# Kernel tuning notes

Measured on AMD Instinct MI355X. Metric: run time of the kernel, lower is better.

The kernel has to match this reference:

```python
import jax, jax.numpy as jnp
from jax import lax
import numpy as np

K = 32          # PyG radius_graph default max_num_neighbors
NEG = -1e9      # mask fill for max-aggregation


def _gather(a, i):  # a [N,C], i [...,] int -> a[i]
    return a[i]


def radius_knn(pos, r):
    # pos [B,N,3] -> (idx [B,N,K], valid [B,N,K]) nearest-K within radius r, self excluded
    sq = jnp.sum(pos * pos, -1)                                   # [B,N]
    d2 = sq[:, :, None] + sq[:, None, :] - 2.0 * jnp.einsum('bnc,bmc->bnm', pos, pos)
    N = pos.shape[1]
    d2 = d2 + jnp.eye(N, dtype=pos.dtype) * 1e9                    # exclude self-loops
    neg, idx = lax.top_k(-d2, K)
    valid = (-neg) <= r * r
    return idx, valid


def fps(pos, n):
    # iterative farthest point sampling, deterministic start at index 0; pos [B,N,3] -> idx [B,n]
    def one(p):
        mind0 = jnp.sum((p - p[0]) ** 2, -1)
        def step(mind, _):
            i = jnp.argmax(mind)
            nd = jnp.sum((p - p[i]) ** 2, -1)
            return jnp.minimum(mind, nd), i
        _, idxs = lax.scan(step, mind0, None, length=n - 1)
        return jnp.concatenate([jnp.zeros((1,), jnp.int32), idxs.astype(jnp.int32)])
    return jax.vmap(one)(pos)


def point_conv(x, pos, idx, valid, W1, b1, W2, b2):
    # PyG PointNetConv: msg = local_nn(concat(x_j, pos_j - pos_i)), max-aggregate
    g = jax.vmap(_gather)
    rel = g(pos, idx) - pos[:, :, None, :]                         # [B,N,K,3]
    feat = rel if x is None else jnp.concatenate([g(x, idx), rel], -1)
    h = jax.nn.relu(feat @ W1 + b1) @ W2 + b2                      # [B,N,K,C]
    h = jnp.where(valid[..., None], h, NEG)
    return jnp.max(h, axis=2)                                      # [B,N,C]


def _forward(pos, W1a, b1a, W1b, b1b, W2a, b2a, W2b, b2b, W3a, b3a, W3b, b3b,
             Wc1, bc1, Wc2, bc2, Wc3, bc3, Wd1, bd1, Wd2, bd2):
    take = jax.vmap(_gather)
    B, N, _ = pos.shape
    idx, v = radius_knn(pos, 0.2)
    x = jax.nn.relu(point_conv(None, pos, idx, v, W1a, b1a, W1b, b1b))
    fi = fps(pos, N // 2)
    x, pos = take(x, fi), take(pos, fi)
    idx, v = radius_knn(pos, 0.4)
    x = jax.nn.relu(point_conv(x, pos, idx, v, W2a, b2a, W2b, b2b))
    fi = fps(pos, N // 8)
    x, pos = take(x, fi), take(pos, fi)
    idx, v = radius_knn(pos, 1.0)
    x = jax.nn.relu(point_conv(x, pos, idx, v, W3a, b3a, W3b, b3b))
    feat = jnp.max(x, axis=1)                                      # global max pool [B,256]
    h = jax.nn.relu(feat @ Wc1 + bc1)
    h = jax.nn.relu(h @ Wc2 + bc2)                                 # dropout is identity in eval
    logits = h @ Wc3 + bc3
    h2 = jax.nn.relu(feat @ Wd1 + bd1)
    d = h2 @ Wd2 + bd2
    return jax.nn.log_softmax(logits, axis=-1), jax.nn.log_softmax(d, axis=-1)


def setup_inputs() -> dict:
    key = jax.random.key(0)
    ks = jax.random.split(key, 32)
    def lin(k, fin, fout):
        kw, kb = jax.random.split(k)
        s = 1.0 / np.sqrt(fin)
        return (jax.random.uniform(kw, (fin, fout), jnp.float32, -s, s),
                jax.random.uniform(kb, (fout,), jnp.float32, -s, s))
    inp = {'pos': jax.random.uniform(ks[0], (8, 4096, 3), jnp.float32)}
    names = [('W1a','b1a',3,64),('W1b','b1b',64,64),('W2a','b2a',67,128),('W2b','b2b',128,128),
             ('W3a','b3a',131,256),('W3b','b3b',256,256),('Wc1','bc1',256,256),('Wc2','bc2',256,256),
             ('Wc3','bc3',256,40),('Wd1','bd1',256,256),('Wd2','bd2',256,2)]
    for i, (wn, bn, fin, fout) in enumerate(names):
        W, b = lin(ks[i + 1], fin, fout)
        inp[wn], inp[bn] = W, b
    return inp


def reference(pos, W1a, b1a, W1b, b1b, W2a, b2a, W2b, b2b, W3a, b3a, W3b, b3b,
              Wc1, bc1, Wc2, bc2, Wc3, bc3, Wd1, bd1, Wd2, bd2):
    return _forward(pos, W1a, b1a, W1b, b1b, W2a, b2a, W2b, b2b, W3a, b3a, W3b, b3b,
                    Wc1, bc1, Wc2, bc2, Wc3, bc3, Wd1, bd1, Wd2, bd2)
```

## Files before the change

### kernel.cpp

```cpp
#include <hip/hip_runtime.h>


#define NB 8

__device__ __forceinline__ unsigned obits(float f) {
  unsigned u = __float_as_uint(f);
  return (u & 0x80000000u) ? ~u : (u | 0x80000000u);
}

static constexpr int CAND = 1024;

template<int CTRL>
__device__ __forceinline__ unsigned long long dpp_max_step(unsigned long long v) {
  const int lo = (int)(unsigned)(v & 0xffffffffull);
  const int hi = (int)(unsigned)(v >> 32);
  const unsigned nlo = (unsigned)__builtin_amdgcn_update_dpp(lo, lo, CTRL, 0xf, 0xf, false);
  const unsigned nhi = (unsigned)__builtin_amdgcn_update_dpp(hi, hi, CTRL, 0xf, 0xf, false);
  const unsigned long long nv = ((unsigned long long)nhi << 32) | nlo;
  return (nv > v) ? nv : v;
}

__device__ __forceinline__ unsigned wave_iscan_add(unsigned x) {
  x += (unsigned)__builtin_amdgcn_update_dpp(0, (int)x, 0x111, 0xf, 0xf, true);
  x += (unsigned)__builtin_amdgcn_update_dpp(0, (int)x, 0x112, 0xf, 0xf, true);
  x += (unsigned)__builtin_amdgcn_update_dpp(0, (int)x, 0x114, 0xf, 0xf, true);
  x += (unsigned)__builtin_amdgcn_update_dpp(0, (int)x, 0x118, 0xf, 0xf, true);
  x += (unsigned)__builtin_amdgcn_update_dpp(0, (int)x, 0x142, 0xa, 0xf, true);
  x += (unsigned)__builtin_amdgcn_update_dpp(0, (int)x, 0x143, 0xc, 0xf, true);
  return x;
}

__device__ __forceinline__ unsigned long long u64max(unsigned long long a,
                                                    unsigned long long b) {
  return (b > a) ? b : a;
}

__device__ __forceinline__ void set_wave_prio_hi() {
#if __has_builtin(__builtin_amdgcn_s_setprio)
  __builtin_amdgcn_s_setprio(3);
#endif
}

__device__ __forceinline__ unsigned morton3_8(unsigned cx, unsigned cy, unsigned cz) {
  unsigned m = ((cx & 1u) << 2) | ((cy & 1u) << 1) | (cz & 1u);
  m |= ((cx & 2u) << 4) | ((cy & 2u) << 3) | ((cz & 2u) << 2);
  m |= ((cx & 4u) << 6) | ((cy & 4u) << 5) | ((cz & 4u) << 4);
  return m;
}

template<int N, int NOUT, int T>
__device__ __forceinline__ void fps_body(char* sm, const float* __restrict__ pb,
                                         int* __restrict__ fi, int b) {
  constexpr int P = N / T;
  constexpr int NW = T / 64;
  constexpr int CELLS = 512;
  constexpr int CH = NOUT;
  constexpr int NCHUNK = N / CH;
  static_assert(CH % P == 0 && N % CH == 0, "chunking");
  static_assert(CELLS <= T, "prefix scan needs CELLS <= T");
  int4* sPosI = (int4*)sm;
  int*  sfi   = (int*)(sm + (size_t)N * 16);
  unsigned long long* sKey =
      (unsigned long long*)(sm + (size_t)N * 16 + NOUT * 4);
  unsigned* hist = (unsigned*)(sm + (size_t)N * 16 + NOUT * 4 + 128);
  int* sOrd = sfi;
  const int tid = threadIdx.x, wid = tid >> 6, lane = tid & 63;
  set_wave_prio_hi();

  for (int t = tid; t < N; t += T) {
    sPosI[t] = make_int4((int)(pb[3*t]   * 8388608.f),
                         (int)(pb[3*t+1] * 8388608.f),
                         (int)(pb[3*t+2] * 8388608.f), 0);
  }
  for (int c = tid; c < CELLS; c += T) hist[c] = 0u;
  __syncthreads();

  unsigned myc[P];
#pragma unroll
  for (int r = 0; r < P; r++) {
    const int t = tid + r * T;
    const int4 p4 = sPosI[t];
    const unsigned cell = morton3_8((unsigned)p4.x >> 20,
                                    (unsigned)p4.y >> 20,
                                    (unsigned)p4.z >> 20);
    myc[r] = cell;
    atomicAdd(&hist[cell], 1u);
  }
  __syncthreads();

  {
    unsigned* sPart = (unsigned*)sKey;
    unsigned v = (tid < CELLS) ? hist[tid] : 0u;
    const unsigned isc = wave_iscan_add(v);
    if (lane == 63) sPart[wid] = isc;
    __syncthreads();
    unsigned offs = 0;
#pragma unroll
    for (int w2 = 0; w2 < NW; w2++) offs += (w2 < wid) ? sPart[w2] : 0u;
    if (tid < CELLS) hist[tid] = offs + isc - v;
    __syncthreads();
  }

  int myslot[P];
#pragma unroll
  for (int r = 0; r < P; r++) myslot[r] = (int)atomicAdd(&hist[myc[r]], 1u);

  int ex[P], ey[P], ez[P]; unsigned einv[P];
  for (int pc = 0; pc < NCHUNK; pc++) {
    __syncthreads();
#pragma unroll
    for (int r = 0; r < P; r++) {
      const int s = myslot[r];
      if (s >= pc * CH && s < (pc + 1) * CH) sOrd[s - pc * CH] = tid + r * T;
    }
    __syncthreads();
    if ((tid * P) / CH == pc) {
#pragma unroll
      for (int e = 0; e < P; e++) {
        const int o = sOrd[tid * P + e - pc * CH];
        const int4 p4 = sPosI[o];
        ex[e] = p4.x; ey[e] = p4.y; ez[e] = p4.z;
        einv[e] = (unsigned)(4095 - o);
      }
    }
  }
  __syncthreads();

  int lox = ex[0], hix = ex[0], loy = ey[0], hiy = ey[0], loz = ez[0], hiz = ez[0];
#pragma unroll
  for (int e = 1; e < P; e++) {
    lox = min(lox, ex[e]); hix = max(hix, ex[e]);
    loy = min(loy, ey[e]); hiy = max(hiy, ey[e]);
    loz = min(loz, ez[e]); hiz = max(hiz, ez[e]);
  }

  const int4 p0 = sPosI[0];
  unsigned long long mind[P];
  unsigned long long bv;
  {
    unsigned long long tv[P];
#pragma unroll
    for (int e = 0; e < P; e++) {
      const long long dx = ex[e] - p0.x, dy = ey[e] - p0.y, dz = ez[e] - p0.z;
      const unsigned long long d2 =
          (unsigned long long)(dx * dx + dy * dy + dz * dz);
      const unsigned long long k = (d2 << 12) | einv[e];
      mind[e] = k; tv[e] = k;
    }
#pragma unroll
    for (int s = 1; s < P; s <<= 1)
#pragma unroll
      for (int e = 0; e + s < P; e += 2 * s)
        if (tv[e + s] > tv[e]) tv[e] = tv[e + s];
    bv = tv[0];
  }
  if (tid == 0) sfi[0] = 0;

  for (int t = 1; t < NOUT; t++) {
    unsigned long long v = bv;
    v = dpp_max_step<0x111>(v);
    v = dpp_max_step<0x112>(v);
    v = dpp_max_step<0x114>(v);
    v = dpp_max_step<0x118>(v);
    v = dpp_max_step<0x142>(v);
    v = dpp_max_step<0x143>(v);
    const int pp = t & 1;
    if (lane == 63) sKey[pp * NW + wid] = v;
    __syncthreads();
    unsigned long long best;
    if (NW == 8) {
      const ulonglong2* sK2 = (const ulonglong2*)(sKey + pp * 8);
      const ulonglong2 a0 = sK2[0], a1 = sK2[1], a2 = sK2[2], a3 = sK2[3];
      best = u64max(u64max(u64max(a0.x, a0.y), u64max(a1.x, a1.y)),
                    u64max(u64max(a2.x, a2.y), u64max(a3.x, a3.y)));
    } else {
      unsigned long long k0 = sKey[pp*NW+0];
#pragma unroll
      for (int w2 = 1; w2 < NW; w2++) k0 = u64max(k0, sKey[pp*NW+w2]);
      best = k0;
    }
    const int ii = 4095 - (int)(best & 0xFFFull);
    if (tid == 0) sfi[t] = ii;
    const int4 wc = sPosI[ii];

    const int ax = max(max(lox - wc.x, wc.x - hix), 0);
    const int ay = max(max(loy - wc.y, wc.y - hiy), 0);
    const int az = max(max(loz - wc.z, wc.z - hiz), 0);
    const unsigned long long lb =
        (unsigned long long)ax * (unsigned long long)ax +
        (unsigned long long)ay * (unsigned long long)ay +
        (unsigned long long)az * (unsigned long long)az;
    if (lb < (bv >> 12)) {
      unsigned long long tv[P];
#pragma unroll
      for (int e = 0; e < P; e++) {
        const long long dx = ex[e] - wc.x, dy = ey[e] - wc.y, dz = ez[e] - wc.z;
        const unsigned long long nd =
            (unsigned long long)(dx * dx + dy * dy + dz * dz);
        const unsigned long long nk = (nd << 12) | einv[e];
        unsigned long long mk = mind[e];
        mk = (nk < mk) ? nk : mk;
        mind[e] = mk;
        tv[e] = mk;
      }
#pragma unroll
      for (int s = 1; s < P; s <<= 1)
#pragma unroll
        for (int e = 0; e + s < P; e += 2 * s)
          if (tv[e + s] > tv[e]) tv[e] = tv[e + s];
      bv = tv[0];
    }
  }
  __syncthreads();
  for (int t = tid; t < NOUT; t += T) fi[(size_t)b * NOUT + t] = sfi[t];
}

template<int N, int H, int C, bool HASX, bool FOLDMAX, int T>
__device__ __forceinline__ void knnconv_body(
    char* sm, const float* __restrict__ pb, int b, int i,
    const float* __restrict__ U, const float* __restrict__ Wrel,
    const float* __restrict__ b1, const float* __restrict__ W2,
    const float* __restrict__ b2, float* __restrict__ out, double rr) {
  constexpr int HCHUNK = (C == 64) ? 64 : (C == 128 ? 32 : 16);
  constexpr int STR = HCHUNK + 4;
  constexpr int NW = T / 64;
  constexpr int EPK = 32 / NW;
  constexpr int BPT = 2048 / T;
  constexpr int KNNFRONT = N * 8 + 13312;
  constexpr int CONVFRONT = 32 * H * 4 + C * STR * 4 + NW * C * 4;
  constexpr int FRONT = (KNNFRONT > CONVFRONT) ? KNNFRONT : CONVFRONT;
  double*   d2s     = (double*)sm;
  unsigned* hist    = (unsigned*)(sm + N * 8);
  int*      candIdx = (int*)(sm + N * 8 + 8192);
  unsigned* sWT     = (unsigned*)(sm + N * 8 + 12288);
  float* h1s  = (float*)sm;
  float* sW2T = (float*)(sm + 32 * H * 4);
  float* sRed = (float*)(sm + 32 * H * 4 + C * STR * 4);
  int*   snbr = (int*)(sm + FRONT);
  float* rel  = (float*)(sm + FRONT + 128);
  int*   pcnt = (int*)(sm + FRONT + 128 + 384);
  int*   pbin = pcnt + 1;
  const int tid = threadIdx.x;

  const double xi = pb[3*i], yi = pb[3*i+1], zi = pb[3*i+2];
  const double si = (xi*xi + yi*yi) + zi*zi;
  for (int t = tid; t < 2048; t += T) hist[t] = 0u;
  if (tid == 0) *pcnt = 0;
  __syncthreads();
  for (int j = tid; j < N; j += T) {
    double xj = pb[3*j], yj = pb[3*j+1], zj = pb[3*j+2];
    double sj = (xj*xj + yj*yj) + zj*zj;
    double dt = (xi*xj + yi*yj) + zi*zj;
    double d2 = (si + sj) - 2.0*dt;
    if (j == i) d2 += 1e9;
    d2s[j] = d2;
    atomicAdd(&hist[obits((float)d2) >> 21], 1u);
  }
  __syncthreads();
  unsigned lsum = 0;
  const int base = tid * BPT;
#pragma unroll
  for (int q = 0; q < BPT; q++) lsum += hist[base + q];
  const unsigned isc = wave_iscan_add(lsum);
  if ((tid & 63) == 63) sWT[tid >> 6] = isc;
  __syncthreads();
  {
    const int wid = tid >> 6;
    unsigned offs = 0;
#pragma unroll
    for (int w2 = 0; w2 < NW; w2++) offs += (w2 < wid) ? sWT[w2] : 0u;
    const unsigned incl = isc + offs, excl = incl - lsum;
    if (excl < 32u && incl >= 32u) {
      unsigned c = excl;
      for (int q = 0; q < BPT; q++) {
        c += hist[base + q];
        if (c >= 32u) { *pbin = base + q; break; }
      }
    }
  }
  __syncthreads();
  const int binT = *pbin;
  for (int j = tid; j < N; j += T) {
    if ((int)(obits((float)d2s[j]) >> 21) <= binT) {
      int p = atomicAdd(pcnt, 1);
      if (p < CAND) candIdx[p] = j;
    }
  }
  __syncthreads();
  const int M = min(*pcnt, CAND);
  for (int c = tid; c < M; c += T) {
    const int j = candIdx[c];
    const double d = d2s[j];
    int rank = 0;
    for (int e = 0; e < M; e++) {
      const int j2 = candIdx[e];
      const double de = d2s[j2];
      rank += (de < d || (de == d && j2 < j)) ? 1 : 0;
    }
    if (rank < 32) snbr[rank] = (d <= rr) ? j : -1;
  }
  __syncthreads();

  if (tid < 32) {
    const int j = snbr[tid];
    float rx = 0.f, ry = 0.f, rz = 0.f;
    if (j >= 0) {
      rx = pb[3*j]   - pb[3*i];
      ry = pb[3*j+1] - pb[3*i+1];
      rz = pb[3*j+2] - pb[3*i+2];
    }
    rel[tid*3+0] = rx; rel[tid*3+1] = ry; rel[tid*3+2] = rz;
  }
  __syncthreads();

  constexpr int QPK = H / 4;
  for (int qi = tid; qi < 32 * QPK; qi += T) {
    const int k = qi / QPK, h0 = (qi - k * QPK) * 4;
    const int j = snbr[k];
    float4 v = make_float4(0.f, 0.f, 0.f, 0.f);
    if (j >= 0) {
      float4 a = HASX ? *(const float4*)&U[((size_t)b * N + j) * H + h0]
                      : *(const float4*)&b1[h0];
      const float rx = rel[k*3], ry = rel[k*3+1], rz = rel[k*3+2];
      const float4 w0 = *(const float4*)&Wrel[h0];
      const float4 w1 = *(const float4*)&Wrel[H + h0];
      const float4 w2 = *(const float4*)&Wrel[2 * H + h0];
      a.x += rx * w0.x + ry * w1.x + rz * w2.x;
      a.y += rx * w0.y + ry * w1.y + rz * w2.y;
      a.z += rx * w0.z + ry * w1.z + rz * w2.z;
      a.w += rx * w0.w + ry * w1.w + rz * w2.w;
      v = make_float4(fmaxf(a.x, 0.f), fmaxf(a.y, 0.f),
                      fmaxf(a.z, 0.f), fmaxf(a.w, 0.f));
    }
    *(float4*)&h1s[k * H + h0] = v;
  }
  const int cc = tid & 63;
  const int kk = tid >> 6;
  constexpr int CC = C / 64;
  float acc[EPK][CC];
#pragma unroll
  for (int e = 0; e < EPK; e++)
#pragma unroll
    for (int q = 0; q < CC; q++) acc[e][q] = 0.f;
  for (int hc = 0; hc < H; hc += HCHUNK) {
    __syncthreads();
    for (int idx = tid; idx < HCHUNK * C; idx += T) {
      const int hh = idx / C, c = idx - hh * C;
      sW2T[c * STR + hh] = W2[(size_t)(hc + hh) * C + c];
    }
    __syncthreads();
    for (int hh0 = 0; hh0 < HCHUNK; hh0 += 4) {
      float4 wv[CC];
#pragma unroll
      for (int q = 0; q < CC; q++)
        wv[q] = *(const float4*)&sW2T[(cc + q * 64) * STR + hh0];
#pragma unroll
      for (int e = 0; e < EPK; e++) {
        const float4 hv = *(const float4*)&h1s[(kk + e * NW) * H + hc + hh0];
#pragma unroll
        for (int q = 0; q < CC; q++) {
          acc[e][q] += hv.x * wv[q].x;
          acc[e][q] += hv.y * wv[q].y;
          acc[e][q] += hv.z * wv[q].z;
          acc[e][q] += hv.w * wv[q].w;
        }
      }
    }
  }
  float m[CC];
#pragma unroll
  for (int q = 0; q < CC; q++) m[q] = -1e9f;
#pragma unroll
  for (int e = 0; e < EPK; e++) {
    if (snbr[kk + e * NW] >= 0) {
#pragma unroll
      for (int q = 0; q < CC; q++) m[q] = fmaxf(m[q], acc[e][q]);
    }
  }
#pragma unroll
  for (int q = 0; q < CC; q++) sRed[kk * C + cc + q * 64] = m[q];
  __syncthreads();
  if (kk == 0) {
#pragma unroll
    for (int q = 0; q < CC; q++) {
      const int c = cc + q * 64;
      float mm = sRed[c];
#pragma unroll
      for (int w2 = 1; w2 < NW; w2++) mm = fmaxf(mm, sRed[w2 * C + c]);
      const float o = (mm > -5e8f) ? (mm + b2[c]) : -1e9f;
      const float r = fmaxf(o, 0.f);
      if (FOLDMAX) {
        atomicMax((int*)&out[b * C + c], __float_as_int(r));
      } else {
        out[((size_t)b * N + i) * C + c] = r;
      }
    }
  }
}

template<int N, int NOUT, int H, int C, bool HASX, int SMSIZE>
__device__ __forceinline__ void stage_fused_impl(
    const float* pos, double rr, int* fi, const float* U, const float* Wrel,
    const float* b1, const float* W2, const float* b2, float* out, char* sm) {
  if (blockIdx.x < NB) {
    fps_body<N, NOUT, 512>(sm, pos + (size_t)blockIdx.x * N * 3, fi, blockIdx.x);
  } else {
    const int row = blockIdx.x - NB;
    const int b = row / N;
    const int i = row - b * N;
    knnconv_body<N, H, C, HASX, false, 512>(sm, pos + (size_t)b * N * 3, b, i,
                                            U, Wrel, b1, W2, b2, out, rr);
  }
}

__global__ __launch_bounds__(512, 2)
void stage1_kernel(const float* __restrict__ pos, double rr, int* __restrict__ fi,
                   const float* __restrict__ Wrel, const float* __restrict__ b1,
                   const float* __restrict__ W2, const float* __restrict__ b2,
                   float* __restrict__ out) {
  __shared__ __align__(16) char sm[75904];
  stage_fused_impl<4096, 2048, 64, 64, false, 75904>(
      pos, rr, fi, nullptr, Wrel, b1, W2, b2, out, sm);
}

__global__ __launch_bounds__(512, 2)
void stage2_kernel(const float* __restrict__ pos, double rr, int* __restrict__ fi,
                   const float* __restrict__ U, const float* __restrict__ Wrel,
                   const float* __restrict__ b1, const float* __restrict__ W2,
                   const float* __restrict__ b2, float* __restrict__ out) {
  __shared__ __align__(16) char sm[39440];
  stage_fused_impl<2048, 512, 128, 128, true, 39440>(
      pos, rr, fi, U, Wrel, b1, W2, b2, out, sm);
}

__global__ __launch_bounds__(512)
void stage3_kernel(const float* __restrict__ pos, double rr,
                   const float* __restrict__ U, const float* __restrict__ Wrel,
                   const float* __restrict__ b1, const float* __restrict__ W2,
                   const float* __restrict__ b2, float* __restrict__ feat) {
  __shared__ __align__(16) char sm[61968];
  const int b = blockIdx.x / 512;
  const int i = blockIdx.x - b * 512;
  knnconv_body<512, 256, 256, true, true, 512>(sm, pos + (size_t)b * 512 * 3,
                                               b, i, U, Wrel, b1, W2, b2,
                                               feat, rr);
}

template<int CIN, int HH>
__global__ __launch_bounds__(HH)
void gp_kernel(const float* __restrict__ X, const float* __restrict__ posPrev,
               const int* __restrict__ fi, int Nprev, int M,
               const float* __restrict__ W, const float* __restrict__ bias,
               float* __restrict__ U, float* __restrict__ posDst) {
  const int row = blockIdx.x;
  const int b = row / M;
  const int tid = threadIdx.x;
  const int j = fi[row];
  __shared__ float sx[CIN];
  if (tid < CIN) sx[tid] = X[((size_t)b * Nprev + j) * CIN + tid];
  if (tid < 3) posDst[(size_t)row * 3 + tid] = posPrev[((size_t)b * Nprev + j) * 3 + tid];
  __syncthreads();
  float a = bias[tid];
  for (int f = 0; f < CIN; f++) a = fmaf(sx[f], W[f * HH + tid], a);
  U[(size_t)row * HH + tid] = a;
}

__global__ __launch_bounds__(256) void head_kernel(
    const float* __restrict__ feat,
    const float* __restrict__ Wc1, const float* __restrict__ bc1,
    const float* __restrict__ Wc2, const float* __restrict__ bc2,
    const float* __restrict__ Wc3, const float* __restrict__ bc3,
    const float* __restrict__ Wd1, const float* __restrict__ bd1,
    const float* __restrict__ Wd2, const float* __restrict__ bd2,
    float* __restrict__ out) {
  const int b = blockIdx.x, tid = threadIdx.x;
  __shared__ float sf[256], sh[256], sh2[256], shd[256], sl[48];
  sf[tid] = feat[b * 256 + tid];
  __syncthreads();
  float a = bc1[tid], ad = bd1[tid];
  for (int f = 0; f < 256; f++) {
    const float fv = sf[f];
    a  = fmaf(fv, Wc1[f * 256 + tid], a);
    ad = fmaf(fv, Wd1[f * 256 + tid], ad);
  }
  sh[tid] = fmaxf(a, 0.f);
  shd[tid] = fmaxf(ad, 0.f);
  __syncthreads();
  float a2 = bc2[tid];
  for (int f = 0; f < 256; f++) a2 = fmaf(sh[f], Wc2[f * 256 + tid], a2);
  sh2[tid] = fmaxf(a2, 0.f);
  __syncthreads();
  if (tid < 40) {
    float l = bc3[tid];
    for (int f = 0; f < 256; f++) l = fmaf(sh2[f], Wc3[f * 40 + tid], l);
    sl[tid] = l;
  }
  if (tid >= 64 && tid < 66) {
    const int q = tid - 64;
    float l = bd2[q];
    for (int f = 0; f < 256; f++) l = fmaf(shd[f], Wd2[f * 2 + q], l);
    sl[40 + q] = l;
  }
  __syncthreads();
  if (tid == 0) {
    float m0 = sl[0];
    for (int q = 1; q < 40; q++) m0 = fmaxf(m0, sl[q]);
    float s = 0.f;
    for (int q = 0; q < 40; q++) s += expf(sl[q] - m0);
    const float ls = logf(s);
    for (int q = 0; q < 40; q++) out[b * 40 + q] = sl[q] - m0 - ls;
    const float m1 = fmaxf(sl[40], sl[41]);
    const float s1 = expf(sl[40] - m1) + expf(sl[41] - m1);
    const float ls1 = logf(s1);
    out[320 + b * 2 + 0] = sl[40] - m1 - ls1;
    out[320 + b * 2 + 1] = sl[41] - m1 - ls1;
  }
}

extern "C" void kernel_launch(void* const* d_in, const int* in_sizes, int n_in,
                              void* d_out, int out_size, void* d_ws, size_t ws_size,
                              hipStream_t stream) {
  (void)in_sizes; (void)n_in; (void)out_size; (void)ws_size;
  const float* pos = (const float*)d_in[0];
  const float* W1a = (const float*)d_in[1];  const float* b1a = (const float*)d_in[2];
  const float* W1b = (const float*)d_in[3];  const float* b1b = (const float*)d_in[4];
  const float* W2a = (const float*)d_in[5];  const float* b2a = (const float*)d_in[6];
  const float* W2b = (const float*)d_in[7];  const float* b2b = (const float*)d_in[8];
  const float* W3a = (const float*)d_in[9];  const float* b3a = (const float*)d_in[10];
  const float* W3b = (const float*)d_in[11]; const float* b3b = (const float*)d_in[12];
  const float* Wc1 = (const float*)d_in[13]; const float* bc1 = (const float*)d_in[14];
  const float* Wc2 = (const float*)d_in[15]; const float* bc2 = (const float*)d_in[16];
  const float* Wc3 = (const float*)d_in[17]; const float* bc3 = (const float*)d_in[18];
  const float* Wd1 = (const float*)d_in[19]; const float* bd1 = (const float*)d_in[20];
  const float* Wd2 = (const float*)d_in[21]; const float* bd2 = (const float*)d_in[22];
  float* out = (float*)d_out;

  char* w = (char*)d_ws;
  auto alloc = [&](size_t bytes) -> void* {
    void* p = (void*)w;
    w += (bytes + 255) & ~(size_t)255;
    return p;
  };
  int*   fi1  = (int*)  alloc((size_t)NB*2048*4);
  float* x1   = (float*)alloc((size_t)NB*4096*64*4);
  float* pos2 = (float*)alloc((size_t)NB*2048*3*4);
  float* U2   = (float*)alloc((size_t)NB*2048*128*4);
  float* x2   = (float*)alloc((size_t)NB*2048*128*4);
  int*   fi2  = (int*)  alloc((size_t)NB*512*4);
  float* pos3 = (float*)alloc((size_t)NB*512*3*4);
  float* U3   = (float*)alloc((size_t)NB*512*256*4);
  float* feat = (float*)alloc((size_t)NB*256*4);

  hipMemsetAsync(feat, 0, (size_t)NB * 256 * 4, stream);

  stage1_kernel<<<NB + NB * 4096, 512, 0, stream>>>(
      pos, 0.2 * 0.2, fi1, W1a, b1a, W1b, b1b, x1);

  gp_kernel<64, 128><<<NB * 2048, 128, 0, stream>>>(
      x1, pos, fi1, 4096, 2048, W2a, b2a, U2, pos2);

  stage2_kernel<<<NB + NB * 2048, 512, 0, stream>>>(
      pos2, 0.4 * 0.4, fi2, U2, W2a + (size_t)64 * 128, b2a, W2b, b2b, x2);

  gp_kernel<128, 256><<<NB * 512, 256, 0, stream>>>(
      x2, pos2, fi2, 2048, 512, W3a, b3a, U3, pos3);

  stage3_kernel<<<NB * 512, 512, 0, stream>>>(
      pos3, 1.0, U3, W3a + (size_t)128 * 256, b3a, W3b, b3b, feat);

  head_kernel<<<NB, 256, 0, stream>>>(feat, Wc1, bc1, Wc2, bc2, Wc3, bc3,
                                      Wd1, bd1, Wd2, bd2, out);
}
```

Baseline: 2.429 ms.

## Run stage-1 FPS for two batches per 1024-thread block to interleave reductions

Stage-1 farthest point sampling now handles two batch elements per block with 1024 threads and 16 waves, interleaving the two independent argmax chains so their DPP reductions and barriers overlap. Positions are stored as packed 3-word arrays to fit two clouds in shared memory. The fused kNN-conv blocks of stage 1 also move to 1024 threads with larger shared memory. The aim is to hide the serial per-iteration latency of FPS, which sits on the critical path. In exchange there are fewer FPS blocks, more registers per thread, and lower occupancy for the conv blocks.

Result: slower. 4.725 ms (+94.5%).

```diff
diff --git a/kernel.cpp b/kernel.cpp
--- a/kernel.cpp
+++ b/kernel.cpp
@@ -2,6 +2,7 @@
 
 
 #define NB 8
+#define NBP 4
 
 __device__ __forceinline__ unsigned obits(float f) {
   unsigned u = __float_as_uint(f);
@@ -46,6 +47,220 @@
   m |= ((cx & 2u) << 4) | ((cy & 2u) << 3) | ((cz & 2u) << 2);
   m |= ((cx & 4u) << 6) | ((cy & 4u) << 5) | ((cz & 4u) << 4);
   return m;
+}
+
+__device__ __forceinline__ unsigned long long tree16(const unsigned long long* sK) {
+  const ulonglong2* k2 = (const ulonglong2*)sK;
+  const ulonglong2 a0 = k2[0], a1 = k2[1], a2 = k2[2], a3 = k2[3],
+                   a4 = k2[4], a5 = k2[5], a6 = k2[6], a7 = k2[7];
+  const unsigned long long m0 = u64max(u64max(a0.x, a0.y), u64max(a1.x, a1.y));
+  const unsigned long long m1 = u64max(u64max(a2.x, a2.y), u64max(a3.x, a3.y));
+  const unsigned long long m2 = u64max(u64max(a4.x, a4.y), u64max(a5.x, a5.y));
+  const unsigned long long m3 = u64max(u64max(a6.x, a6.y), u64max(a7.x, a7.y));
+  return u64max(u64max(m0, m1), u64max(m2, m3));
+}
+
+template<int N, int NOUT, int T, int P>
+__device__ __forceinline__ unsigned long long fps_init_one(
+    const float* __restrict__ pb, unsigned* __restrict__ sPos,
+    int* __restrict__ sOrd, unsigned* __restrict__ hist,
+    unsigned* __restrict__ sPart,
+    int (&ex)[P], int (&ey)[P], int (&ez)[P], unsigned (&einv)[P],
+    unsigned long long (&mind)[P], int (&bb)[6]) {
+  constexpr int NW = T / 64;
+  constexpr int CELLS = 512;
+  constexpr int CH = NOUT;
+  constexpr int NCHUNK = N / CH;
+  static_assert(N == 4096 && CELLS <= T && N % CH == 0, "pair cfg");
+  const int tid = threadIdx.x, wid = tid >> 6, lane = tid & 63;
+  for (int t = tid; t < N; t += T) {
+    sPos[3*t]   = (unsigned)(int)(pb[3*t]   * 8388608.f);
+    sPos[3*t+1] = (unsigned)(int)(pb[3*t+1] * 8388608.f);
+    sPos[3*t+2] = (unsigned)(int)(pb[3*t+2] * 8388608.f);
+  }
+  for (int c = tid; c < CELLS; c += T) hist[c] = 0u;
+  __syncthreads();
+  unsigned myc[P];
+#pragma unroll
+  for (int r = 0; r < P; r++) {
+    const int t = tid + r * T;
+    const unsigned cell = morton3_8(sPos[3*t] >> 20, sPos[3*t+1] >> 20,
+                                    sPos[3*t+2] >> 20);
+    myc[r] = cell;
+    atomicAdd(&hist[cell], 1u);
+  }
+  __syncthreads();
+  {
+    unsigned v = (tid < CELLS) ? hist[tid] : 0u;
+    const unsigned isc = wave_iscan_add(v);
+    if (lane == 63) sPart[wid] = isc;
+    __syncthreads();
+    unsigned offs = 0;
+#pragma unroll
+    for (int w2 = 0; w2 < NW; w2++) offs += (w2 < wid) ? sPart[w2] : 0u;
+    if (tid < CELLS) hist[tid] = offs + isc - v;
+    __syncthreads();
+  }
+  int myslot[P];
+#pragma unroll
+  for (int r = 0; r < P; r++) myslot[r] = (int)atomicAdd(&hist[myc[r]], 1u);
+  for (int pc = 0; pc < NCHUNK; pc++) {
+    __syncthreads();
+#pragma unroll
+    for (int r = 0; r < P; r++) {
+      const int s = myslot[r];
+      if (s >= pc * CH && s < (pc + 1) * CH) sOrd[s - pc * CH] = tid + r * T;
+    }
+    __syncthreads();
+    if ((tid * P) / CH == pc) {
+#pragma unroll
+      for (int e = 0; e < P; e++) {
+        const int o = sOrd[tid * P + e - pc * CH];
+        ex[e] = (int)sPos[3*o]; ey[e] = (int)sPos[3*o+1]; ez[e] = (int)sPos[3*o+2];
+        einv[e] = (unsigned)(4095 - o);
+      }
+    }
+  }
+  __syncthreads();
+  bb[0] = ex[0]; bb[1] = ex[0]; bb[2] = ey[0];
+  bb[3] = ey[0]; bb[4] = ez[0]; bb[5] = ez[0];
+#pragma unroll
+  for (int e = 1; e < P; e++) {
+    bb[0] = min(bb[0], ex[e]); bb[1] = max(bb[1], ex[e]);
+    bb[2] = min(bb[2], ey[e]); bb[3] = max(bb[3], ey[e]);
+    bb[4] = min(bb[4], ez[e]); bb[5] = max(bb[5], ez[e]);
+  }
+  const int x0 = (int)sPos[0], y0 = (int)sPos[1], z0 = (int)sPos[2];
+  unsigned long long tv[P];
+#pragma unroll
+  for (int e = 0; e < P; e++) {
+    const long long dx = ex[e] - x0, dy = ey[e] - y0, dz = ez[e] - z0;
+    const unsigned long long d2 =
+        (unsigned long long)(dx * dx + dy * dy + dz * dz);
+    const unsigned long long k = (d2 << 12) | einv[e];
+    mind[e] = k; tv[e] = k;
+  }
+#pragma unroll
+  for (int s = 1; s < P; s <<= 1)
+#pragma unroll
+    for (int e = 0; e + s < P; e += 2 * s)
+      if (tv[e + s] > tv[e]) tv[e] = tv[e + s];
+  return tv[0];
+}
+
+template<int N, int NOUT, int T>
+__device__ __forceinline__ void fps_pair_body(char* sm, const float* __restrict__ pos,
+                                              int* __restrict__ fi, int bA, int bB) {
+  constexpr int P = N / T;
+  constexpr int NW = T / 64;
+  unsigned* sPosA = (unsigned*)sm;
+  unsigned* sPosB = (unsigned*)(sm + (size_t)N * 12);
+  int* sfiA = (int*)(sm + (size_t)N * 24);
+  int* sfiB = (int*)(sm + (size_t)N * 24 + NOUT * 4);
+  unsigned long long* sKeyA =
+      (unsigned long long*)(sm + (size_t)N * 24 + NOUT * 8);
+  unsigned long long* sKeyB = sKeyA + 2 * NW;
+  unsigned* hist = (unsigned*)(sm + (size_t)N * 24 + NOUT * 8 + 4 * NW * 8);
+  int* sOrd = sfiA;
+  unsigned* sPart = (unsigned*)sKeyA;
+  const int tid = threadIdx.x, lane = tid & 63, wid = tid >> 6;
+  set_wave_prio_hi();
+
+  int exA[P], eyA[P], ezA[P]; unsigned einvA[P];
+  unsigned long long mindA[P]; int bbA[6];
+  int exB[P], eyB[P], ezB[P]; unsigned einvB[P];
+  unsigned long long mindB[P]; int bbB[6];
+  unsigned long long bvA = fps_init_one<N, NOUT, T, P>(
+      pos + (size_t)bA * N * 3, sPosA, sOrd, hist, sPart,
+      exA, eyA, ezA, einvA, mindA, bbA);
+  unsigned long long bvB = fps_init_one<N, NOUT, T, P>(
+      pos + (size_t)bB * N * 3, sPosB, sOrd, hist, sPart,
+      exB, eyB, ezB, einvB, mindB, bbB);
+  __syncthreads();
+  if (tid == 0) { sfiA[0] = 0; sfiB[0] = 0; }
+
+  for (int t = 1; t < NOUT; t++) {
+    unsigned long long vA = bvA, vB = bvB;
+    vA = dpp_max_step<0x111>(vA); vB = dpp_max_step<0x111>(vB);
+    vA = dpp_max_step<0x112>(vA); vB = dpp_max_step<0x112>(vB);
+    vA = dpp_max_step<0x114>(vA); vB = dpp_max_step<0x114>(vB);
+    vA = dpp_max_step<0x118>(vA); vB = dpp_max_step<0x118>(vB);
+    vA = dpp_max_step<0x142>(vA); vB = dpp_max_step<0x142>(vB);
+    vA = dpp_max_step<0x143>(vA); vB = dpp_max_step<0x143>(vB);
+    const int pp = t & 1;
+    if (lane == 63) { sKeyA[pp * NW + wid] = vA; sKeyB[pp * NW + wid] = vB; }
+    __syncthreads();
+    const unsigned long long bestA = tree16(sKeyA + pp * NW);
+    const unsigned long long bestB = tree16(sKeyB + pp * NW);
+    const int iiA = 4095 - (int)(bestA & 0xFFFull);
+    const int iiB = 4095 - (int)(bestB & 0xFFFull);
+    if (tid == 0) { sfiA[t] = iiA; sfiB[t] = iiB; }
+    const int wAx = (int)sPosA[3*iiA], wAy = (int)sPosA[3*iiA+1],
+              wAz = (int)sPosA[3*iiA+2];
+    const int wBx = (int)sPosB[3*iiB], wBy = (int)sPosB[3*iiB+1],
+              wBz = (int)sPosB[3*iiB+2];
+    {
+      const int ax = max(max(bbA[0] - wAx, wAx - bbA[1]), 0);
+      const int ay = max(max(bbA[2] - wAy, wAy - bbA[3]), 0);
+      const int az = max(max(bbA[4] - wAz, wAz - bbA[5]), 0);
+      const unsigned long long lb =
+          (unsigned long long)ax * (unsigned long long)ax +
+          (unsigned long long)ay * (unsigned long long)ay +
+          (unsigned long long)az * (unsigned long long)az;
+      if (lb < (bvA >> 12)) {
+        unsigned long long tv[P];
+#pragma unroll
+        for (int e = 0; e < P; e++) {
+          const long long dx = exA[e] - wAx, dy = eyA[e] - wAy, dz = ezA[e] - wAz;
+          const unsigned long long nd =
+              (unsigned long long)(dx * dx + dy * dy + dz * dz);
+          const unsigned long long nk = (nd << 12) | einvA[e];
+          unsigned long long mk = mindA[e];
+          mk = (nk < mk) ? nk : mk;
+          mindA[e] = mk; tv[e] = mk;
+        }
+#pragma unroll
+        for (int s = 1; s < P; s <<= 1)
+#pragma unroll
+          for (int e = 0; e + s < P; e += 2 * s)
+            if (tv[e + s] > tv[e]) tv[e] = tv[e + s];
+        bvA = tv[0];
+      }
+    }
+    {
+      const int ax = max(max(bbB[0] - wBx, wBx - bbB[1]), 0);
+      const int ay = max(max(bbB[2] - wBy, wBy - bbB[3]), 0);
+      const int az = max(max(bbB[4] - wBz, wBz - bbB[5]), 0);
+      const unsigned long long lb =
+          (unsigned long long)ax * (unsigned long long)ax +
+          (unsigned long long)ay * (unsigned long long)ay +
+          (unsigned long long)az * (unsigned long long)az;
+      if (lb < (bvB >> 12)) {
+        unsigned long long tv[P];
+#pragma unroll
+        for (int e = 0; e < P; e++) {
+          const long long dx = exB[e] - wBx, dy = eyB[e] - wBy, dz = ezB[e] - wBz;
+          const unsigned long long nd =
+              (unsigned long long)(dx * dx + dy * dy + dz * dz);
+          const unsigned long long nk = (nd << 12) | einvB[e];
+          unsigned long long mk = mindB[e];
+          mk = (nk < mk) ? nk : mk;
+          mindB[e] = mk; tv[e] = mk;
+        }
+#pragma unroll
+        for (int s = 1; s < P; s <<= 1)
+#pragma unroll
+          for (int e = 0; e + s < P; e += 2 * s)
+            if (tv[e + s] > tv[e]) tv[e] = tv[e + s];
+        bvB = tv[0];
+      }
+    }
+  }
+  __syncthreads();
+  for (int t = tid; t < NOUT; t += T) {
+    fi[(size_t)bA * NOUT + t] = sfiA[t];
+    fi[(size_t)bB * NOUT + t] = sfiB[t];
+  }
 }
 
 template<int N, int NOUT, int T>
@@ -74,7 +289,6 @@
   }
   for (int c = tid; c < CELLS; c += T) hist[c] = 0u;
   __syncthreads();
-
   unsigned myc[P];
 #pragma unroll
   for (int r = 0; r < P; r++) {
@@ -87,7 +301,6 @@
     atomicAdd(&hist[cell], 1u);
   }
   __syncthreads();
-
   {
     unsigned* sPart = (unsigned*)sKey;
     unsigned v = (tid < CELLS) ? hist[tid] : 0u;
@@ -100,11 +313,9 @@
     if (tid < CELLS) hist[tid] = offs + isc - v;
     __syncthreads();
   }
-
   int myslot[P];
 #pragma unroll
   for (int r = 0; r < P; r++) myslot[r] = (int)atomicAdd(&hist[myc[r]], 1u);
-
   int ex[P], ey[P], ez[P]; unsigned einv[P];
   for (int pc = 0; pc < NCHUNK; pc++) {
     __syncthreads();
@@ -125,7 +336,6 @@
     }
   }
   __syncthreads();
-
   int lox = ex[0], hix = ex[0], loy = ey[0], hiy = ey[0], loz = ez[0], hiz = ez[0];
 #pragma unroll
   for (int e = 1; e < P; e++) {
@@ -133,7 +343,6 @@
     loy = min(loy, ey[e]); hiy = max(hiy, ey[e]);
     loz = min(loz, ez[e]); hiz = max(hiz, ez[e]);
   }
-
   const int4 p0 = sPosI[0];
   unsigned long long mind[P];
   unsigned long long bv;
@@ -155,7 +364,6 @@
     bv = tv[0];
   }
   if (tid == 0) sfi[0] = 0;
-
   for (int t = 1; t < NOUT; t++) {
     unsigned long long v = bv;
     v = dpp_max_step<0x111>(v);
@@ -182,7 +390,6 @@
     const int ii = 4095 - (int)(best & 0xFFFull);
     if (tid == 0) sfi[t] = ii;
     const int4 wc = sPosI[ii];
-
     const int ax = max(max(lox - wc.x, wc.x - hix), 0);
     const int ay = max(max(loy - wc.y, wc.y - hiy), 0);
     const int az = max(max(loz - wc.z, wc.z - hiz), 0);
@@ -398,7 +605,25 @@
   }
 }
 
-template<int N, int NOUT, int H, int C, bool HASX, int SMSIZE>
+__global__ __launch_bounds__(1024)
+void stage1_kernel(const float* __restrict__ pos, double rr, int* __restrict__ fi,
+                   const float* __restrict__ Wrel, const float* __restrict__ b1,
+                   const float* __restrict__ W2, const float* __restrict__ b2,
+                   float* __restrict__ out) {
+  __shared__ __align__(16) char sm[117248];
+  if (blockIdx.x < NBP) {
+    fps_pair_body<4096, 2048, 1024>(sm, pos, fi,
+                                    2 * blockIdx.x, 2 * blockIdx.x + 1);
+  } else {
+    const int row = blockIdx.x - NBP;
+    const int b = row >> 12;
+    const int i = row & 4095;
+    knnconv_body<4096, 64, 64, false, false, 1024>(
+        sm, pos + (size_t)b * 4096 * 3, b, i, nullptr, Wrel, b1, W2, b2, out, rr);
+  }
+}
+
+template<int N, int NOUT, int H, int C, bool HASX>
 __device__ __forceinline__ void stage_fused_impl(
     const float* pos, double rr, int* fi, const float* U, const float* Wrel,
     const float* b1, const float* W2, const float* b2, float* out, char* sm) {
@@ -414,22 +639,12 @@
 }
 
 __global__ __launch_bounds__(512, 2)
-void stage1_kernel(const float* __restrict__ pos, double rr, int* __restrict__ fi,
-                   const float* __restrict__ Wrel, const float* __restrict__ b1,
-                   const float* __restrict__ W2, const float* __restrict__ b2,
-                   float* __restrict__ out) {
-  __shared__ __align__(16) char sm[75904];
-  stage_fused_impl<4096, 2048, 64, 64, false, 75904>(
-      pos, rr, fi, nullptr, Wrel, b1, W2, b2, out, sm);
-}
-
-__global__ __launch_bounds__(512, 2)
 void stage2_kernel(const float* __restrict__ pos, double rr, int* __restrict__ fi,
                    const float* __restrict__ U, const float* __restrict__ Wrel,
                    const float* __restrict__ b1, const float* __restrict__ W2,
                    const float* __restrict__ b2, float* __restrict__ out) {
   __shared__ __align__(16) char sm[39440];
-  stage_fused_impl<2048, 512, 128, 128, true, 39440>(
+  stage_fused_impl<2048, 512, 128, 128, true>(
       pos, rr, fi, U, Wrel, b1, W2, b2, out, sm);
 }
 
@@ -553,7 +768,7 @@
 
   hipMemsetAsync(feat, 0, (size_t)NB * 256 * 4, stream);
 
-  stage1_kernel<<<NB + NB * 4096, 512, 0, stream>>>(
+  stage1_kernel<<<NBP + NB * 4096, 1024, 0, stream>>>(
       pos, 0.2 * 0.2, fi1, W1a, b1a, W1b, b1b, x1);
 
   gp_kernel<64, 128><<<NB * 2048, 128, 0, stream>>>(
```
